# Performance work log

Measured on AMD Instinct MI355X. Metric: run time of the kernel, lower is better.

Reference implementation:

```python
import jax, jax.numpy as jnp
import numpy as np

N = 8192        # number of cells/nodes
D_IN = 30       # input feature dim
P_DIM = 3       # position dim
HID = 32        # attention hidden dim
D_OUT = 30      # backbone output dim
FF = 128        # MLP hidden width
SIGMA = 0.3     # spatial decay sigma


def setup_inputs() -> dict:
    key = jax.random.key(0)
    ks = jax.random.split(key, 12)
    w = lambda k, shape: (jax.random.normal(k, shape, jnp.float32) * 0.1)
    return {
        "t": jax.random.uniform(ks[0], (1,), jnp.float32),
        "Z": jax.random.normal(ks[1], (N, D_IN + P_DIM + 1), jnp.float32),
        # SpatialAttentionLayer params (Q/K/V projections + output proj)
        "Wq": w(ks[2], (D_IN, HID)), "bq": jnp.zeros((HID,), jnp.float32),
        "Wk": w(ks[3], (D_IN, HID)), "bk": jnp.zeros((HID,), jnp.float32),
        "Wv": w(ks[4], (D_IN, HID)), "bv": jnp.zeros((HID,), jnp.float32),
        "Wo": w(ks[5], (HID, D_OUT)), "bo": jnp.zeros((D_OUT,), jnp.float32),
        # LayerNorm
        "ln_g": jnp.ones((D_OUT,), jnp.float32), "ln_b": jnp.zeros((D_OUT,), jnp.float32),
        # backbone MLP: Linear(30,128) -> SiLU -> Linear(128,30)
        "W1": w(ks[6], (D_OUT, FF)), "b1": jnp.zeros((FF,), jnp.float32),
        "W2": w(ks[7], (FF, D_OUT)), "b2": jnp.zeros((D_OUT,), jnp.float32),
        # expr_head: Linear(30,30)
        "We": w(ks[8], (D_OUT, D_OUT)), "be": jnp.zeros((D_OUT,), jnp.float32),
    }


def reference(t, Z, Wq, bq, Wk, bk, Wv, bv, Wo, bo, ln_g, ln_b, W1, b1, W2, b2, We, be):
    # Z: (N, D_IN + P_DIM + 1); last column is kinetic energy (unused in fwd)
    X = Z[:, :-1]                       # (N, 33)
    P = X[:, -P_DIM:]                   # (N, 3) positions
    F = X[:, :D_IN]                     # (N, 30) features

    # --- SpatialAttentionLayer: sigma distance-decay attention, no softmax ---
    Q = F @ Wq + bq
    K = F @ Wk + bk
    V = F @ Wv + bv
    scores = (Q @ K.T) / jnp.sqrt(jnp.float32(HID))          # (N, N)
    pn = jnp.sum(P * P, axis=1)
    d2 = jnp.maximum(pn[:, None] + pn[None, :] - 2.0 * (P @ P.T), 0.0)
    decay = jnp.exp(-d2 / (2.0 * SIGMA * SIGMA))              # spatial decay kernel
    A = jax.nn.sigmoid(scores) * decay                        # no-softmax attention
    A = A / (jnp.sum(A, axis=1, keepdims=True) + 1e-8)        # row-normalized message passing
    H = (A @ V) @ Wo + bo                                     # (N, D_OUT)

    # --- LayerNorm(output_dim) ---
    mu = jnp.mean(H, axis=-1, keepdims=True)
    var = jnp.mean((H - mu) ** 2, axis=-1, keepdims=True)
    Hn = (H - mu) * jax.lax.rsqrt(var + 1e-5) * ln_g + ln_b

    # --- Linear(30,128) -> SiLU -> Linear(128,30) ---
    H2 = jax.nn.silu(Hn @ W1 + b1) @ W2 + b2

    # --- expr_head ---
    feature_velo = H2 @ We + be                               # (N, 30)

    # static_pos=True -> zero position velocities (velocity_head bypassed)
    pos_velo = jnp.zeros_like(P)                              # (N, 3)

    # kinetic energy term
    ke = 0.5 * jnp.mean(feature_velo ** 2, axis=1) + 0.5 * jnp.mean(pos_velo ** 2, axis=1)
    return jnp.concatenate([feature_velo, pos_velo, ke[:, None]], axis=1)  # (N, 34)
```

## Files before the change

kernel.cpp:

```cpp
#include <hip/hip_runtime.h>
#include <hip/hip_bf16.h>

#define N      8192
#define D_IN   30
#define HID    32
#define D_OUT  30
#define FFD    128
#define ZC     34
#define JGC    16

typedef __attribute__((ext_vector_type(8))) short short8;
typedef __attribute__((ext_vector_type(16))) float f32x16;

static __device__ __forceinline__ ushort f2bf(float x) {
    uint32_t u = __float_as_uint(x);
    uint32_t r = (u + 0x7fffu + ((u >> 16) & 1u)) >> 16;
    return (ushort)r;
}
static __device__ __forceinline__ float bf2f(ushort u) {
    return __uint_as_float(((uint32_t)u) << 16);
}

__global__ __launch_bounds__(256) void dv_qkv_kernel(
    const float* __restrict__ Z,
    const float* __restrict__ Wq, const float* __restrict__ bq,
    const float* __restrict__ Wk, const float* __restrict__ bk,
    const float* __restrict__ Wv, const float* __restrict__ bv,
    const float* __restrict__ Wo,
    const float* __restrict__ W2, const float* __restrict__ We,
    const float* __restrict__ b2, const float* __restrict__ be,
    ushort* __restrict__ Qb, ushort* __restrict__ Kb,
    ushort* __restrict__ VWot, ushort* __restrict__ KA,
    ushort* __restrict__ QB, float* __restrict__ W2e, float* __restrict__ b2e)
{
    __shared__ ushort sv[8][33];
    const int t = blockIdx.x * 256 + threadIdx.x;
    const int i = t >> 5;
    const int h = t & 31;
    const float* z = Z + (size_t)i * ZC;

    float q = bq[h], k = bk[h], v = bv[h];
#pragma unroll
    for (int d = 0; d < D_IN; ++d) {
        float zf = z[d];
        q = fmaf(zf, Wq[d * HID + h], q);
        k = fmaf(zf, Wk[d * HID + h], k);
        v = fmaf(zf, Wv[d * HID + h], v);
    }
    const float QS = 0.17677669529663687f * 1.4426950408889634f;
    Qb[(size_t)i * HID + h] = f2bf(q * QS);
    Kb[(size_t)i * HID + h] = f2bf(k);
    sv[threadIdx.x >> 5][h] = f2bf(v);

    if (h == 0) {
        float p0 = z[D_IN], p1 = z[D_IN + 1], p2 = z[D_IN + 2];
        const float C2 = 1.4426950408889634f / 0.18f;
        const float SC = sqrtf(2.0f * C2);
        float px = p0 * SC, py = p1 * SC, pz = p2 * SC;
        float w  = -C2 * (p0 * p0 + p1 * p1 + p2 * p2);
        ushort phx = f2bf(px), phy = f2bf(py), phz = f2bf(pz);
        ushort plx = f2bf(px - bf2f(phx));
        ushort ply = f2bf(py - bf2f(phy));
        ushort plz = f2bf(pz - bf2f(phz));
        ushort wh  = f2bf(w);
        ushort wl  = f2bf(w - bf2f(wh));
        ushort nhx = phx ^ 0x8000, nhy = phy ^ 0x8000, nhz = phz ^ 0x8000;
        ushort nlx = plx ^ 0x8000, nly = ply ^ 0x8000, nlz = plz ^ 0x8000;
        ushort nwh = wh ^ 0x8000,  nwl = wl ^ 0x8000;
        const ushort one = 0x3F80, none = 0xBF80;
        ushort ka0[8] = {nwh, nwl, none, none, nhx, nhy, nhz, nhx};
        ushort ka1[8] = {nhy, nhz, nlx, nly, nlz, nlx, nly, nlz};
        ushort qb0[8] = {one, one, wh, wl, phx, phy, phz, plx};
        ushort qb1[8] = {ply, plz, phx, phy, phz, plx, ply, plz};
        *(uint4*)&KA[(size_t)i * 8]       = *(uint4*)ka0;
        *(uint4*)&KA[((size_t)N + i) * 8] = *(uint4*)ka1;
        *(uint4*)&QB[(size_t)i * 8]       = *(uint4*)qb0;
        *(uint4*)&QB[((size_t)N + i) * 8] = *(uint4*)qb1;
    }

    if (blockIdx.x < 15) {
        int idx = blockIdx.x * 256 + threadIdx.x;
        int f = idx / 30, o = idx - f * 30;
        float acc = 0.f;
#pragma unroll
        for (int d = 0; d < D_OUT; ++d)
            acc = fmaf(W2[f * D_OUT + d], We[d * D_OUT + o], acc);
        W2e[idx] = acc;
        if (idx < D_OUT) {
            float a2 = be[idx];
#pragma unroll
            for (int d = 0; d < D_OUT; ++d)
                a2 = fmaf(b2[d], We[d * D_OUT + idx], a2);
            b2e[idx] = a2;
        }
    }

    __syncthreads();
    const int io = threadIdx.x >> 5, c = threadIdx.x & 31;
    const int ii = blockIdx.x * 8 + io;
    float val;
    if (c < 30) {
        float acc = 0.f;
#pragma unroll
        for (int hh = 0; hh < HID; ++hh)
            acc = fmaf(bf2f(sv[io][hh]), Wo[hh * D_OUT + c], acc);
        val = acc;
    } else {
        val = (c == 31) ? 1.0f : 0.f;
    }
    VWot[(size_t)c * N + ii] = f2bf(val);
}

__global__ __launch_bounds__(256, 2) void dv_attn_kernel(
    const ushort* __restrict__ Qb, const ushort* __restrict__ Kb,
    const ushort* __restrict__ VWot, const ushort* __restrict__ KA,
    const ushort* __restrict__ QB, float* __restrict__ partial, int nch)
{
    __shared__ ushort lK[128 * 32];
    __shared__ ushort lV[32 * 128];
    __shared__ ushort lKA[2][128 * 8];

    const int tid  = threadIdx.x;
    const int lane = tid & 63;
    const int wv   = tid >> 6;
    const int h2   = lane >> 5;
    const int l31  = lane & 31;
    const int rb   = blockIdx.x & 63;
    const int jg   = blockIdx.x >> 6;
    const int i0w  = rb * 128 + wv * 32;

    const ushort* qp = Qb + (size_t)(i0w + l31) * HID + h2 * 8;
    const short8 qf0 = *(const short8*)qp;
    const short8 qf1 = *(const short8*)(qp + 16);
    const short8 qaug = *(const short8*)&QB[((size_t)h2 * N + i0w + l31) * 8];

    f32x16 zacc, oacc;
#pragma unroll
    for (int r = 0; r < 16; ++r) { zacc[r] = 0.f; oacc[r] = 0.f; }

    const int cA0 = (h2 + (l31 >> 1)) & 3;
    const int cA1 = (cA0 + 2) & 3;

    for (int ch = 0; ch < nch; ++ch) {
        const int j0 = (jg * nch + ch) << 7;
        __syncthreads();
        {
            int idx = tid;
#pragma unroll
            for (int rep = 0; rep < 2; ++rep, idx += 256) {
                int jr = idx >> 2, cc = idx & 3;
                int c2 = (cc + (jr >> 1)) & 3;
                *(uint4*)&lK[jr * 32 + c2 * 8] =
                    *(const uint4*)&Kb[(size_t)(j0 + jr) * HID + cc * 8];
            }
            idx = tid;
#pragma unroll
            for (int rep = 0; rep < 4; ++rep, idx += 256) {
                int hh = idx >> 5, cc = idx & 31;
                int cs = cc ^ hh;
                *(uint2*)&lV[hh * 128 + cs * 4] =
                    *(const uint2*)&VWot[(size_t)hh * N + j0 + cc * 4];
            }
            {
                int half = tid >> 7, jj = tid & 127;
                *(uint4*)&lKA[half][jj * 8] =
                    *(const uint4*)&KA[((size_t)half * N + j0 + jj) * 8];
            }
        }
        __syncthreads();

#pragma unroll
        for (int t32 = 0; t32 < 4; ++t32) {
            const ushort* krow = &lK[(t32 * 32 + l31) * 32];
            short8 kf0 = *(const short8*)&krow[cA0 * 8];
            short8 kf1 = *(const short8*)&krow[cA1 * 8];
            f32x16 s = __builtin_amdgcn_mfma_f32_32x32x16_bf16(kf0, qf0, zacc, 0, 0, 0);
            s = __builtin_amdgcn_mfma_f32_32x32x16_bf16(kf1, qf1, s, 0, 0, 0);

            short8 kaug = *(const short8*)&lKA[h2][(t32 * 32 + l31) * 8];
            f32x16 gA = __builtin_amdgcn_mfma_f32_32x32x16_bf16(kaug, qaug, zacc, 0, 0, 0);

            uint32_t pk[8];
#pragma unroll
            for (int p = 0; p < 8; ++p) {
                float d0 = fmaxf(gA[2 * p], 0.f);
                float d1 = fmaxf(gA[2 * p + 1], 0.f);
                float eg0 = __builtin_amdgcn_exp2f(-d0);
                float es0 = __builtin_amdgcn_exp2f(-s[2 * p]);
                float a0  = eg0 * __builtin_amdgcn_rcpf(1.0f + es0);
                float eg1 = __builtin_amdgcn_exp2f(-d1);
                float es1 = __builtin_amdgcn_exp2f(-s[2 * p + 1]);
                float a1  = eg1 * __builtin_amdgcn_rcpf(1.0f + es1);
                asm("v_cvt_pk_bf16_f32 %0, %1, %2" : "=v"(pk[p]) : "v"(a0), "v"(a1));
            }
            union BV { uint32_t u[4]; short8 v; };
            BV fa, fb;
            fa.u[0] = pk[0]; fa.u[1] = pk[1]; fa.u[2] = pk[2]; fa.u[3] = pk[3];
            fb.u[0] = pk[4]; fb.u[1] = pk[5]; fb.u[2] = pk[6]; fb.u[3] = pk[7];

            const ushort* vrow = &lV[l31 * 128];
            const int cb = t32 * 8 + h2;
            BV b0, b1;
            *(uint2*)&b0.u[0] = *(const uint2*)&vrow[((cb    ) ^ l31) * 4];
            *(uint2*)&b0.u[2] = *(const uint2*)&vrow[((cb + 2) ^ l31) * 4];
            *(uint2*)&b1.u[0] = *(const uint2*)&vrow[((cb + 4) ^ l31) * 4];
            *(uint2*)&b1.u[2] = *(const uint2*)&vrow[((cb + 6) ^ l31) * 4];

            oacc = __builtin_amdgcn_mfma_f32_32x32x16_bf16(fa.v, b0.v, oacc, 0, 0, 0);
            oacc = __builtin_amdgcn_mfma_f32_32x32x16_bf16(fb.v, b1.v, oacc, 0, 0, 0);
        }
    }

#pragma unroll
    for (int r = 0; r < 16; ++r) {
        int ir = (r & 3) + 8 * (r >> 2) + 4 * h2 + i0w;
        partial[(size_t)ir * (JGC * 32) + jg * 32 + l31] = oacc[r];
    }
}

__global__ __launch_bounds__(256) void dv_epilogue_kernel(
    const float* __restrict__ partial,
    const float* __restrict__ bo,
    const float* __restrict__ ln_g, const float* __restrict__ ln_b,
    const float* __restrict__ W1, const float* __restrict__ b1,
    const float* __restrict__ W2e, const float* __restrict__ b2e,
    float* __restrict__ out)
{
    __shared__ float sr [32 * 16];
    __shared__ float sHl[30 * 16];
    __shared__ float sHn[30 * 16];
    __shared__ float shf[128 * 16];
    __shared__ float sker[16 * 16];

    const int tid  = threadIdx.x;
    const int row0 = blockIdx.x * 16;

#pragma unroll
    for (int rep = 0; rep < 2; ++rep) {
        int idx = tid + rep * 256;
        int r = idx >> 5, c = idx & 31;
        const float* pp = partial + (size_t)(row0 + r) * (JGC * 32) + c;
        float s = 0.f;
#pragma unroll
        for (int jg = 0; jg < JGC; ++jg)
            s += pp[jg * 32];
        sr[c * 16 + r] = s;
    }
    __syncthreads();

    const int rl  = tid & 15, grp = tid >> 4;
    const int o0  = grp * 2;
    const bool g15 = grp < 15;

    if (g15) {
        float inv = __builtin_amdgcn_rcpf(sr[31 * 16 + rl] + 1e-8f);
        float2 bb = *(const float2*)&bo[o0];
        sHl[(o0    ) * 16 + rl] = fmaf(sr[(o0    ) * 16 + rl], inv, bb.x);
        sHl[(o0 + 1) * 16 + rl] = fmaf(sr[(o0 + 1) * 16 + rl], inv, bb.y);
    }
    __syncthreads();

    if (tid < 16) {
        const int r = tid;
        float mu = 0.f;
#pragma unroll
        for (int o = 0; o < D_OUT; ++o) mu += sHl[o * 16 + r];
        mu *= (1.0f / D_OUT);
        float var = 0.f;
#pragma unroll
        for (int o = 0; o < D_OUT; ++o) {
            float d = sHl[o * 16 + r] - mu; var = fmaf(d, d, var);
        }
        float rs = rsqrtf(var * (1.0f / D_OUT) + 1e-5f);
#pragma unroll
        for (int o = 0; o < D_OUT; ++o)
            sHn[o * 16 + r] = fmaf((sHl[o * 16 + r] - mu) * rs, ln_g[o], ln_b[o]);
    }
    __syncthreads();

    {
        const int f0 = grp * 8;
        float acc[8];
        float4 b4a = *(const float4*)&b1[f0];
        float4 b4b = *(const float4*)&b1[f0 + 4];
        acc[0] = b4a.x; acc[1] = b4a.y; acc[2] = b4a.z; acc[3] = b4a.w;
        acc[4] = b4b.x; acc[5] = b4b.y; acc[6] = b4b.z; acc[7] = b4b.w;
#pragma unroll
        for (int o = 0; o < D_OUT; ++o) {
            float4 wa = *(const float4*)&W1[o * FFD + f0];
            float4 wb = *(const float4*)&W1[o * FFD + f0 + 4];
            float hn = sHn[o * 16 + rl];
            acc[0] = fmaf(hn, wa.x, acc[0]); acc[1] = fmaf(hn, wa.y, acc[1]);
            acc[2] = fmaf(hn, wa.z, acc[2]); acc[3] = fmaf(hn, wa.w, acc[3]);
            acc[4] = fmaf(hn, wb.x, acc[4]); acc[5] = fmaf(hn, wb.y, acc[5]);
            acc[6] = fmaf(hn, wb.z, acc[6]); acc[7] = fmaf(hn, wb.w, acc[7]);
        }
        const float L2E = 1.4426950408889634f;
#pragma unroll
        for (int ff = 0; ff < 8; ++ff) {
            float a = acc[ff];
            shf[(f0 + ff) * 16 + rl] =
                a * __builtin_amdgcn_rcpf(1.0f + __builtin_amdgcn_exp2f(-a * L2E));
        }
    }
    __syncthreads();

    if (g15) {
        float2 bb = *(const float2*)&b2e[o0];
        float a0 = bb.x, a1 = bb.y;
#pragma unroll 8
        for (int f = 0; f < FFD; ++f) {
            float2 w = *(const float2*)&W2e[f * D_OUT + o0];
            float hf = shf[f * 16 + rl];
            a0 = fmaf(hf, w.x, a0); a1 = fmaf(hf, w.y, a1);
        }
        float* op = out + (size_t)(row0 + rl) * ZC;
        op[o0] = a0; op[o0 + 1] = a1;
        sker[grp * 16 + rl] = fmaf(a0, a0, a1 * a1);
    }
    __syncthreads();

    if (tid < 16) {
        float ke = 0.f;
#pragma unroll
        for (int g = 0; g < 15; ++g) ke += sker[g * 16 + tid];
        float* op = out + (size_t)(row0 + tid) * ZC;
        op[30] = 0.f; op[31] = 0.f; op[32] = 0.f;
        op[33] = ke * (0.5f / D_OUT);
    }
}

extern "C" void kernel_launch(void* const* d_in, const int* in_sizes, int n_in,
                              void* d_out, int out_size, void* d_ws, size_t ws_size,
                              hipStream_t stream)
{
    const float* Z  = (const float*)d_in[1];
    const float* Wq = (const float*)d_in[2];
    const float* bq = (const float*)d_in[3];
    const float* Wk = (const float*)d_in[4];
    const float* bk = (const float*)d_in[5];
    const float* Wv = (const float*)d_in[6];
    const float* bv = (const float*)d_in[7];
    const float* Wo = (const float*)d_in[8];
    const float* bo = (const float*)d_in[9];
    const float* lg = (const float*)d_in[10];
    const float* lb = (const float*)d_in[11];
    const float* W1 = (const float*)d_in[12];
    const float* b1 = (const float*)d_in[13];
    const float* W2 = (const float*)d_in[14];
    const float* b2 = (const float*)d_in[15];
    const float* We = (const float*)d_in[16];
    const float* be = (const float*)d_in[17];
    float* out = (float*)d_out;

    ushort* Qb   = (ushort*)d_ws;
    ushort* Kb   = Qb + (size_t)N * HID;
    ushort* VWot = Kb + (size_t)N * HID;
    ushort* KA   = VWot + (size_t)N * HID;
    ushort* QB   = KA + (size_t)N * 16;
    float*  W2e  = (float*)(QB + (size_t)N * 16);
    float*  b2e  = W2e + FFD * D_OUT;
    float*  partial = b2e + 32;

    int nch = N / (JGC * 128);

    hipLaunchKernelGGL(dv_qkv_kernel, dim3((N * HID) / 256), dim3(256), 0, stream,
                       Z, Wq, bq, Wk, bk, Wv, bv, Wo, W2, We, b2, be,
                       Qb, Kb, VWot, KA, QB, W2e, b2e);
    hipLaunchKernelGGL(dv_attn_kernel, dim3(64 * JGC), dim3(256), 0, stream,
                       Qb, Kb, VWot, KA, QB, partial, nch);
    hipLaunchKernelGGL(dv_epilogue_kernel, dim3(N / 16), dim3(256), 0, stream,
                       partial, bo, lg, lb, W1, b1, W2e, b2e, out);
}
```

Baseline: 63.85 us.

## Double attention j-split, restructure epilogue to warp-per-row with transposed weights

Doubles the number of j-column groups in the attention kernel, which gives twice as many blocks, each covering half the key chunks, at the cost of a larger partial buffer and more reduction work in the epilogue. The epilogue is rewritten so each 32-lane group handles one row: LayerNorm statistics come from shuffle reductions, and both MLP matmuls read pre-transposed W1t/W2eT weights (produced in the qkv kernel) as contiguous float4 dot products. The clamp of the squared distance to zero before exp2 is removed. That can let tiny negative rounding values give exp slightly above one.

Result: slower. 76.15 us (+19.3%).

```diff
diff --git a/kernel.cpp b/kernel.cpp
--- a/kernel.cpp
+++ b/kernel.cpp
@@ -7,7 +7,7 @@
 #define D_OUT  30
 #define FFD    128
 #define ZC     34
-#define JGC    16
+#define JGC    32
 
 typedef __attribute__((ext_vector_type(8))) short short8;
 typedef __attribute__((ext_vector_type(16))) float f32x16;
@@ -27,11 +27,13 @@
     const float* __restrict__ Wk, const float* __restrict__ bk,
     const float* __restrict__ Wv, const float* __restrict__ bv,
     const float* __restrict__ Wo,
-    const float* __restrict__ W2, const float* __restrict__ We,
+    const float* __restrict__ W1, const float* __restrict__ W2,
+    const float* __restrict__ We,
     const float* __restrict__ b2, const float* __restrict__ be,
     ushort* __restrict__ Qb, ushort* __restrict__ Kb,
     ushort* __restrict__ VWot, ushort* __restrict__ KA,
-    ushort* __restrict__ QB, float* __restrict__ W2e, float* __restrict__ b2e)
+    ushort* __restrict__ QB,
+    float* __restrict__ W1t, float* __restrict__ W2eT, float* __restrict__ b2e)
 {
     __shared__ ushort sv[8][33];
     const int t = blockIdx.x * 256 + threadIdx.x;
@@ -80,12 +82,12 @@
 
     if (blockIdx.x < 15) {
         int idx = blockIdx.x * 256 + threadIdx.x;
-        int f = idx / 30, o = idx - f * 30;
+        int o = idx >> 7, f = idx & 127;
         float acc = 0.f;
 #pragma unroll
         for (int d = 0; d < D_OUT; ++d)
             acc = fmaf(W2[f * D_OUT + d], We[d * D_OUT + o], acc);
-        W2e[idx] = acc;
+        W2eT[o * FFD + f] = acc;
         if (idx < D_OUT) {
             float a2 = be[idx];
 #pragma unroll
@@ -93,6 +95,11 @@
                 a2 = fmaf(b2[d], We[d * D_OUT + idx], a2);
             b2e[idx] = a2;
         }
+    }
+    if (blockIdx.x >= 16 && blockIdx.x < 32) {
+        int idx = (blockIdx.x - 16) * 256 + threadIdx.x;
+        int f = idx >> 5, o = idx & 31;
+        W1t[idx] = (o < D_OUT) ? W1[o * FFD + f] : 0.f;
     }
 
     __syncthreads();
@@ -183,12 +190,10 @@
             uint32_t pk[8];
 #pragma unroll
             for (int p = 0; p < 8; ++p) {
-                float d0 = fmaxf(gA[2 * p], 0.f);
-                float d1 = fmaxf(gA[2 * p + 1], 0.f);
-                float eg0 = __builtin_amdgcn_exp2f(-d0);
+                float eg0 = __builtin_amdgcn_exp2f(-gA[2 * p]);
                 float es0 = __builtin_amdgcn_exp2f(-s[2 * p]);
                 float a0  = eg0 * __builtin_amdgcn_rcpf(1.0f + es0);
-                float eg1 = __builtin_amdgcn_exp2f(-d1);
+                float eg1 = __builtin_amdgcn_exp2f(-gA[2 * p + 1]);
                 float es1 = __builtin_amdgcn_exp2f(-s[2 * p + 1]);
                 float a1  = eg1 * __builtin_amdgcn_rcpf(1.0f + es1);
                 asm("v_cvt_pk_bf16_f32 %0, %1, %2" : "=v"(pk[p]) : "v"(a0), "v"(a1));
@@ -222,111 +227,91 @@
     const float* __restrict__ partial,
     const float* __restrict__ bo,
     const float* __restrict__ ln_g, const float* __restrict__ ln_b,
-    const float* __restrict__ W1, const float* __restrict__ b1,
-    const float* __restrict__ W2e, const float* __restrict__ b2e,
+    const float* __restrict__ W1t, const float* __restrict__ b1,
+    const float* __restrict__ W2eT, const float* __restrict__ b2e,
     float* __restrict__ out)
 {
-    __shared__ float sr [32 * 16];
-    __shared__ float sHl[30 * 16];
-    __shared__ float sHn[30 * 16];
-    __shared__ float shf[128 * 16];
-    __shared__ float sker[16 * 16];
+    __shared__ float sHn[8][32];
+    __shared__ float shf[8][128];
 
     const int tid  = threadIdx.x;
-    const int row0 = blockIdx.x * 16;
-
-#pragma unroll
-    for (int rep = 0; rep < 2; ++rep) {
-        int idx = tid + rep * 256;
-        int r = idx >> 5, c = idx & 31;
-        const float* pp = partial + (size_t)(row0 + r) * (JGC * 32) + c;
-        float s = 0.f;
+    const int row  = tid >> 5;
+    const int c    = tid & 31;
+    const int grow = blockIdx.x * 8 + row;
+    const bool a30 = c < 30;
+    const int  c30 = a30 ? c : 0;
+
+    float sv = 0.f;
+    {
+        const float* pp = partial + (size_t)grow * (JGC * 32) + c;
 #pragma unroll
         for (int jg = 0; jg < JGC; ++jg)
-            s += pp[jg * 32];
-        sr[c * 16 + r] = s;
-    }
+            sv += pp[jg * 32];
+    }
+    float rsum = __shfl(sv, 31, 32);
+    float inv  = __builtin_amdgcn_rcpf(rsum + 1e-8f);
+    float Hl   = a30 ? fmaf(sv, inv, bo[c30]) : 0.f;
+
+    float x = Hl;
+#pragma unroll
+    for (int m = 1; m < 32; m <<= 1) x += __shfl_xor(x, m, 32);
+    float mu = x * (1.0f / D_OUT);
+    float d  = a30 ? (Hl - mu) : 0.f;
+    float v2 = d * d;
+#pragma unroll
+    for (int m = 1; m < 32; m <<= 1) v2 += __shfl_xor(v2, m, 32);
+    float rs = rsqrtf(v2 * (1.0f / D_OUT) + 1e-5f);
+    float Hn = a30 ? fmaf(d * rs, ln_g[c30], ln_b[c30]) : 0.f;
+    sHn[row][c] = Hn;
     __syncthreads();
 
-    const int rl  = tid & 15, grp = tid >> 4;
-    const int o0  = grp * 2;
-    const bool g15 = grp < 15;
-
-    if (g15) {
-        float inv = __builtin_amdgcn_rcpf(sr[31 * 16 + rl] + 1e-8f);
-        float2 bb = *(const float2*)&bo[o0];
-        sHl[(o0    ) * 16 + rl] = fmaf(sr[(o0    ) * 16 + rl], inv, bb.x);
-        sHl[(o0 + 1) * 16 + rl] = fmaf(sr[(o0 + 1) * 16 + rl], inv, bb.y);
+    {
+        const float4* hn4 = (const float4*)&sHn[row][0];
+        const float L2E = 1.4426950408889634f;
+#pragma unroll
+        for (int k = 0; k < 4; ++k) {
+            const int f = c + 32 * k;
+            const float4* w4 = (const float4*)&W1t[f * 32];
+            float acc = b1[f];
+#pragma unroll
+            for (int e = 0; e < 8; ++e) {
+                float4 hh = hn4[e], ww = w4[e];
+                acc = fmaf(hh.x, ww.x, acc);
+                acc = fmaf(hh.y, ww.y, acc);
+                acc = fmaf(hh.z, ww.z, acc);
+                acc = fmaf(hh.w, ww.w, acc);
+            }
+            shf[row][f] = acc *
+                __builtin_amdgcn_rcpf(1.0f + __builtin_amdgcn_exp2f(-acc * L2E));
+        }
     }
     __syncthreads();
 
-    if (tid < 16) {
-        const int r = tid;
-        float mu = 0.f;
-#pragma unroll
-        for (int o = 0; o < D_OUT; ++o) mu += sHl[o * 16 + r];
-        mu *= (1.0f / D_OUT);
-        float var = 0.f;
-#pragma unroll
-        for (int o = 0; o < D_OUT; ++o) {
-            float d = sHl[o * 16 + r] - mu; var = fmaf(d, d, var);
-        }
-        float rs = rsqrtf(var * (1.0f / D_OUT) + 1e-5f);
-#pragma unroll
-        for (int o = 0; o < D_OUT; ++o)
-            sHn[o * 16 + r] = fmaf((sHl[o * 16 + r] - mu) * rs, ln_g[o], ln_b[o]);
-    }
-    __syncthreads();
-
+    float val = 0.f, kep = 0.f;
     {
-        const int f0 = grp * 8;
-        float acc[8];
-        float4 b4a = *(const float4*)&b1[f0];
-        float4 b4b = *(const float4*)&b1[f0 + 4];
-        acc[0] = b4a.x; acc[1] = b4a.y; acc[2] = b4a.z; acc[3] = b4a.w;
-        acc[4] = b4b.x; acc[5] = b4b.y; acc[6] = b4b.z; acc[7] = b4b.w;
-#pragma unroll
-        for (int o = 0; o < D_OUT; ++o) {
-            float4 wa = *(const float4*)&W1[o * FFD + f0];
-            float4 wb = *(const float4*)&W1[o * FFD + f0 + 4];
-            float hn = sHn[o * 16 + rl];
-            acc[0] = fmaf(hn, wa.x, acc[0]); acc[1] = fmaf(hn, wa.y, acc[1]);
-            acc[2] = fmaf(hn, wa.z, acc[2]); acc[3] = fmaf(hn, wa.w, acc[3]);
-            acc[4] = fmaf(hn, wb.x, acc[4]); acc[5] = fmaf(hn, wb.y, acc[5]);
-            acc[6] = fmaf(hn, wb.z, acc[6]); acc[7] = fmaf(hn, wb.w, acc[7]);
-        }
-        const float L2E = 1.4426950408889634f;
-#pragma unroll
-        for (int ff = 0; ff < 8; ++ff) {
-            float a = acc[ff];
-            shf[(f0 + ff) * 16 + rl] =
-                a * __builtin_amdgcn_rcpf(1.0f + __builtin_amdgcn_exp2f(-a * L2E));
-        }
-    }
-    __syncthreads();
-
-    if (g15) {
-        float2 bb = *(const float2*)&b2e[o0];
-        float a0 = bb.x, a1 = bb.y;
-#pragma unroll 8
-        for (int f = 0; f < FFD; ++f) {
-            float2 w = *(const float2*)&W2e[f * D_OUT + o0];
-            float hf = shf[f * 16 + rl];
-            a0 = fmaf(hf, w.x, a0); a1 = fmaf(hf, w.y, a1);
-        }
-        float* op = out + (size_t)(row0 + rl) * ZC;
-        op[o0] = a0; op[o0 + 1] = a1;
-        sker[grp * 16 + rl] = fmaf(a0, a0, a1 * a1);
-    }
-    __syncthreads();
-
-    if (tid < 16) {
-        float ke = 0.f;
-#pragma unroll
-        for (int g = 0; g < 15; ++g) ke += sker[g * 16 + tid];
-        float* op = out + (size_t)(row0 + tid) * ZC;
+        const float4* h4 = (const float4*)&shf[row][0];
+        const float4* w4 = (const float4*)&W2eT[c30 * FFD];
+        float acc = 0.f;
+#pragma unroll
+        for (int q = 0; q < 32; ++q) {
+            float4 hh = h4[q], ww = w4[q];
+            acc = fmaf(hh.x, ww.x, acc);
+            acc = fmaf(hh.y, ww.y, acc);
+            acc = fmaf(hh.z, ww.z, acc);
+            acc = fmaf(hh.w, ww.w, acc);
+        }
+        val = acc + b2e[c30];
+        if (a30) {
+            out[(size_t)grow * ZC + c] = val;
+            kep = val * val;
+        }
+    }
+#pragma unroll
+    for (int m = 1; m < 32; m <<= 1) kep += __shfl_xor(kep, m, 32);
+    if (c == 0) {
+        float* op = out + (size_t)grow * ZC;
         op[30] = 0.f; op[31] = 0.f; op[32] = 0.f;
-        op[33] = ke * (0.5f / D_OUT);
+        op[33] = kep * (0.5f / D_OUT);
     }
 }
 
@@ -358,17 +343,18 @@
     ushort* VWot = Kb + (size_t)N * HID;
     ushort* KA   = VWot + (size_t)N * HID;
     ushort* QB   = KA + (size_t)N * 16;
-    float*  W2e  = (float*)(QB + (size_t)N * 16);
-    float*  b2e  = W2e + FFD * D_OUT;
+    float*  W1t  = (float*)(QB + (size_t)N * 16);
+    float*  W2eT = W1t + FFD * 32;
+    float*  b2e  = W2eT + D_OUT * FFD;
     float*  partial = b2e + 32;
 
     int nch = N / (JGC * 128);
 
     hipLaunchKernelGGL(dv_qkv_kernel, dim3((N * HID) / 256), dim3(256), 0, stream,
-                       Z, Wq, bq, Wk, bk, Wv, bv, Wo, W2, We, b2, be,
-                       Qb, Kb, VWot, KA, QB, W2e, b2e);
+                       Z, Wq, bq, Wk, bk, Wv, bv, Wo, W1, W2, We, b2, be,
+                       Qb, Kb, VWot, KA, QB, W1t, W2eT, b2e);
     hipLaunchKernelGGL(dv_attn_kernel, dim3(64 * JGC), dim3(256), 0, stream,
                        Qb, Kb, VWot, KA, QB, partial, nch);
-    hipLaunchKernelGGL(dv_epilogue_kernel, dim3(N / 16), dim3(256), 0, stream,
-                       partial, bo, lg, lb, W1, b1, W2e, b2e, out);
-}
+    hipLaunchKernelGGL(dv_epilogue_kernel, dim3(N / 8), dim3(256), 0, stream,
+                       partial, bo, lg, lb, W1t, b1, W2eT, b2e, out);
+}
```
